# Kernel optimization log

Hardware: AMD Instinct MI355X
Metric: run time of the kernel (lower is better)

The kernel has to match this reference:

```python
import jax, jax.numpy as jnp
import numpy as np

N_NODES = 50000


def setup_inputs() -> dict:
    key = jax.random.key(0)
    k1, k2, k3, k4, k5 = jax.random.split(key, 5)
    h = jax.random.normal(k1, (50000, 256), dtype=jnp.float32)
    norm = jax.random.uniform(k2, (50000, 1), dtype=jnp.float32)
    weight = jax.random.normal(k3, (256, 96), dtype=jnp.float32) * (1.0 / np.sqrt(96.0))
    src = jax.random.randint(k4, (800000,), 0, N_NODES, dtype=jnp.int64)
    dst = jax.random.randint(k5, (800000,), 0, N_NODES, dtype=jnp.int64)
    return {"h": h, "norm": norm, "weight": weight, "src": src, "dst": dst}


def reference(h, norm, weight, src, dst):
    # dense projection: [N, in] @ [in, out] -> [N, out]
    hw = jnp.matmul(h, weight)
    # pre-aggregation degree norm
    hw = hw * norm
    # copy_src + sum: gather messages from src, scatter-add into dst
    msgs = hw[src]  # [E, out]
    agg = jax.ops.segment_sum(msgs, dst, num_segments=N_NODES)
    # post-aggregation degree norm + activation
    out = jax.nn.relu(agg * norm)
    return out
```

## Files before the change

### kernel.cpp

```cpp
#include <hip/hip_runtime.h>

#define M_NODES 50000
#define KDIM    256
#define NDIM    96
#define NEDGE   800000
#define BM      128
#define GEMM_BLKS 391
#define NPB     64
#define NBUCK   782
#define CAPB    1536
#define EPB     2048
#define NBLK_SC 391

typedef short bf16x8 __attribute__((ext_vector_type(8)));
typedef float f32x4  __attribute__((ext_vector_type(4)));

__device__ inline unsigned short f2bf(float x) {
    unsigned u = __float_as_uint(x);
    u = (u + 0x7fffu + ((u >> 16) & 1u)) >> 16;
    return (unsigned short)u;
}
__device__ inline unsigned pack2bf(float x, float y) {
    return (unsigned)f2bf(x) | ((unsigned)f2bf(y) << 16);
}

__global__ __launch_bounds__(256) void prep_w_kernel(
    const float* __restrict__ w, unsigned short* __restrict__ wt,
    int* __restrict__ gcursor)
{
    if (blockIdx.x == 0)
        for (int i = threadIdx.x; i < NBUCK; i += 256)
            gcursor[i] = i * CAPB;
    int i = blockIdx.x * 256 + threadIdx.x;
    if (i < KDIM * NDIM) {
        int n = i >> 8;
        int k = i & 255;
        wt[i] = f2bf(w[(size_t)k * NDIM + n]);
    }
}

__global__ __launch_bounds__(256) void fused_gemm_scatter_kernel(
    const float* __restrict__ h, const float* __restrict__ norm,
    const unsigned short* __restrict__ wt, unsigned short* __restrict__ hwb,
    const int* __restrict__ src, const int* __restrict__ dst,
    int* __restrict__ gcursor, unsigned* __restrict__ binned)
{
    __shared__ __align__(16) char smem[96 * 512];

    const int tid = threadIdx.x;

    if (blockIdx.x < GEMM_BLKS) {
        unsigned short* w_lds = reinterpret_cast<unsigned short*>(smem);
        const int lane = tid & 63;
        const int wv   = tid >> 6;
        const int row0 = blockIdx.x * BM;

#pragma unroll
        for (int it = 0; it < 12; ++it) {
            int idx = tid + it * 256;
            int n   = idx >> 5;
            int kb  = (idx & 31) * 16;
            uint4 v = *reinterpret_cast<const uint4*>(
                reinterpret_cast<const char*>(wt) + n * 512 + kb);
            *reinterpret_cast<uint4*>(
                reinterpret_cast<char*>(w_lds) + n * 512 + (kb ^ ((n & 7) << 4))) = v;
        }
        __syncthreads();

        f32x4 acc0[6], acc1[6];
#pragma unroll
        for (int f = 0; f < 6; ++f) {
            acc0[f] = (f32x4){0.f, 0.f, 0.f, 0.f};
            acc1[f] = (f32x4){0.f, 0.f, 0.f, 0.f};
        }

        const int ar = wv * 16 + (lane & 15);
        const int kg = lane >> 4;
        int arow0 = row0 + ar;
        int arow1 = row0 + ar + 64;
        if (arow0 >= M_NODES) arow0 = M_NODES - 1;
        if (arow1 >= M_NODES) arow1 = M_NODES - 1;
        const float* __restrict__ hr0 = h + (size_t)arow0 * KDIM;
        const float* __restrict__ hr1 = h + (size_t)arow1 * KDIM;

#pragma unroll
        for (int s = 0; s < 8; ++s) {
            const int k0 = s * 32 + kg * 8;
            float4 p0 = *reinterpret_cast<const float4*>(hr0 + k0);
            float4 q0 = *reinterpret_cast<const float4*>(hr0 + k0 + 4);
            float4 p1 = *reinterpret_cast<const float4*>(hr1 + k0);
            float4 q1 = *reinterpret_cast<const float4*>(hr1 + k0 + 4);
            union { bf16x8 v; unsigned u[4]; } a0, a1;
            a0.u[0] = pack2bf(p0.x, p0.y); a0.u[1] = pack2bf(p0.z, p0.w);
            a0.u[2] = pack2bf(q0.x, q0.y); a0.u[3] = pack2bf(q0.z, q0.w);
            a1.u[0] = pack2bf(p1.x, p1.y); a1.u[1] = pack2bf(p1.z, p1.w);
            a1.u[2] = pack2bf(q1.x, q1.y); a1.u[3] = pack2bf(q1.z, q1.w);

            const int kb = s * 64 + kg * 16;
#pragma unroll
            for (int f = 0; f < 6; ++f) {
                int n = f * 16 + (lane & 15);
                bf16x8 b = *reinterpret_cast<const bf16x8*>(
                    reinterpret_cast<const char*>(w_lds) + n * 512 + (kb ^ ((n & 7) << 4)));
                acc0[f] = __builtin_amdgcn_mfma_f32_16x16x32_bf16(a0.v, b, acc0[f], 0, 0, 0);
                acc1[f] = __builtin_amdgcn_mfma_f32_16x16x32_bf16(a1.v, b, acc1[f], 0, 0, 0);
            }
        }

        const int crow = wv * 16 + (lane >> 4) * 4;
        const int ccol = lane & 15;
#pragma unroll
        for (int r = 0; r < 4; ++r) {
            int rowA = row0 + crow + r;
            if (rowA < M_NODES) {
                float nv = norm[rowA];
#pragma unroll
                for (int f = 0; f < 6; ++f)
                    hwb[(size_t)rowA * NDIM + f * 16 + ccol] = f2bf(acc0[f][r] * nv);
            }
            int rowB = rowA + 64;
            if (rowB < M_NODES) {
                float nv = norm[rowB];
#pragma unroll
                for (int f = 0; f < 6; ++f)
                    hwb[(size_t)rowB * NDIM + f * 16 + ccol] = f2bf(acc1[f][r] * nv);
            }
        }
    } else {
        int* cnt  = reinterpret_cast<int*>(smem);
        int* base = cnt + NBUCK;
        const int blk = blockIdx.x - GEMM_BLKS;
        const int e0 = blk * EPB;
        const int e1 = (e0 + EPB < NEDGE) ? e0 + EPB : NEDGE;

        for (int i = tid; i < NBUCK; i += 256) cnt[i] = 0;
        __syncthreads();
        for (int e = e0 + tid; e < e1; e += 256)
            atomicAdd(&cnt[dst[e] >> 6], 1);
        __syncthreads();
        for (int i = tid; i < NBUCK; i += 256) {
            int c = cnt[i];
            base[i] = c ? atomicAdd(&gcursor[i], c) : 0;
        }
        __syncthreads();
        for (int i = tid; i < NBUCK; i += 256) cnt[i] = 0;
        __syncthreads();
        for (int e = e0 + tid; e < e1; e += 256) {
            int d = dst[e];
            int b = d >> 6;
            int pos = base[b] + atomicAdd(&cnt[b], 1);
            if (pos < (b + 1) * CAPB)
                binned[pos] = ((unsigned)(d & 63) << 16) | (unsigned)src[e];
        }
    }
}

#define ACCV(A, v)                                     \
    A[0] += __uint_as_float((v).x << 16);              \
    A[1] += __uint_as_float((v).x & 0xffff0000u);      \
    A[2] += __uint_as_float((v).y << 16);              \
    A[3] += __uint_as_float((v).y & 0xffff0000u);      \
    A[4] += __uint_as_float((v).z << 16);              \
    A[5] += __uint_as_float((v).z & 0xffff0000u);      \
    A[6] += __uint_as_float((v).w << 16);              \
    A[7] += __uint_as_float((v).w & 0xffff0000u);

__global__ __launch_bounds__(256) void csr_agg_kernel(
    const unsigned* __restrict__ binned, const int* __restrict__ gcursor,
    const unsigned short* __restrict__ hwb, const float* __restrict__ norm,
    float* __restrict__ out)
{
    __shared__ unsigned eL[CAPB];
    __shared__ unsigned short oL[CAPB];
    __shared__ int cnt[NPB];
    __shared__ int pfxE[NPB];

    const int b  = blockIdx.x;
    const int t  = threadIdx.x;
    const int e0 = b * CAPB;
    int cntE = gcursor[b] - e0;
    if (cntE > CAPB) cntE = CAPB;

    for (int i = t; i < cntE; i += 256) eL[i] = binned[e0 + i];
    if (t < NPB) cnt[t] = 0;
    __syncthreads();
    for (int i = t; i < cntE; i += 256)
        atomicAdd(&cnt[(eL[i] >> 16) & 63], 1);
    __syncthreads();
    if (t < NPB) pfxE[t] = cnt[t];
    __syncthreads();
    for (int st = 1; st < NPB; st <<= 1) {
        int o = (t >= st && t < NPB) ? pfxE[t - st] : 0;
        __syncthreads();
        if (t < NPB) pfxE[t] += o;
        __syncthreads();
    }
    if (t < NPB) {
        int ex = pfxE[t] - cnt[t];
        pfxE[t] = ex;
        cnt[t]  = ex;
    }
    __syncthreads();
    for (int i = t; i < cntE; i += 256) {
        unsigned v = eL[i];
        int d = (v >> 16) & 63;
        int p = atomicAdd(&cnt[d], 1);
        oL[p] = (unsigned short)(v & 0xffffu);
    }
    __syncthreads();

#pragma unroll
    for (int pass = 0; pass < 3; ++pass) {
        const int u     = pass * 256 + t;
        const int node  = u / 12;
        const int c8    = u - node * 12;
        const int gnode = b * NPB + node;
        if (gnode < M_NODES) {
            const int s0 = pfxE[node];
            const int s1 = cnt[node];
            float acc[8]  = {0.f, 0.f, 0.f, 0.f, 0.f, 0.f, 0.f, 0.f};
            float acc2[8] = {0.f, 0.f, 0.f, 0.f, 0.f, 0.f, 0.f, 0.f};
            int e = s0;
            for (; e + 4 <= s1; e += 4) {
                int a0 = oL[e], a1 = oL[e + 1], a2 = oL[e + 2], a3 = oL[e + 3];
                uint4 v0 = *reinterpret_cast<const uint4*>(hwb + (size_t)a0 * NDIM + c8 * 8);
                uint4 v1 = *reinterpret_cast<const uint4*>(hwb + (size_t)a1 * NDIM + c8 * 8);
                uint4 v2 = *reinterpret_cast<const uint4*>(hwb + (size_t)a2 * NDIM + c8 * 8);
                uint4 v3 = *reinterpret_cast<const uint4*>(hwb + (size_t)a3 * NDIM + c8 * 8);
                ACCV(acc, v0); ACCV(acc2, v1); ACCV(acc, v2); ACCV(acc2, v3);
            }
            for (; e < s1; ++e) {
                int a0 = oL[e];
                uint4 v0 = *reinterpret_cast<const uint4*>(hwb + (size_t)a0 * NDIM + c8 * 8);
                ACCV(acc, v0);
            }
            const float nv = norm[gnode];
            float4 o0, o1;
            o0.x = fmaxf((acc[0] + acc2[0]) * nv, 0.f);
            o0.y = fmaxf((acc[1] + acc2[1]) * nv, 0.f);
            o0.z = fmaxf((acc[2] + acc2[2]) * nv, 0.f);
            o0.w = fmaxf((acc[3] + acc2[3]) * nv, 0.f);
            o1.x = fmaxf((acc[4] + acc2[4]) * nv, 0.f);
            o1.y = fmaxf((acc[5] + acc2[5]) * nv, 0.f);
            o1.z = fmaxf((acc[6] + acc2[6]) * nv, 0.f);
            o1.w = fmaxf((acc[7] + acc2[7]) * nv, 0.f);
            float4* po = reinterpret_cast<float4*>(out + (size_t)gnode * NDIM + c8 * 8);
            po[0] = o0; po[1] = o1;
        }
    }
}

extern "C" void kernel_launch(void* const* d_in, const int* in_sizes, int n_in,
                              void* d_out, int out_size, void* d_ws, size_t ws_size,
                              hipStream_t stream)
{
    const float* h    = (const float*)d_in[0];
    const float* norm = (const float*)d_in[1];
    const float* w    = (const float*)d_in[2];
    const int*   src  = (const int*)d_in[3];
    const int*   dst  = (const int*)d_in[4];
    float* out = (float*)d_out;

    unsigned short* hwb = (unsigned short*)d_ws;
    unsigned short* wt  = hwb + (size_t)M_NODES * NDIM;
    int* gcursor = (int*)(wt + KDIM * NDIM);
    unsigned* binned = (unsigned*)(gcursor + 800);

    prep_w_kernel<<<(KDIM * NDIM + 255) / 256, 256, 0, stream>>>(w, wt, gcursor);
    fused_gemm_scatter_kernel<<<GEMM_BLKS + NBLK_SC, 256, 0, stream>>>(
        h, norm, wt, hwb, src, dst, gcursor, binned);
    csr_agg_kernel<<<NBUCK, 256, 0, stream>>>(binned, gcursor, hwb, norm, out);
}
```

Before: 70.36 us.

## Halve GEMM tile, read weights from global instead of LDS, shuffle-based prefix scan

The GEMM branch now processes 64 rows per block instead of 128 and launches twice as many GEMM blocks. It drops the LDS weight staging and syncthreads, reading bf16 weight fragments directly from global memory (L2/L1 cached). All h row loads are issued up front into registers. The binning branch gets smaller dedicated shared arrays, which may raise occupancy, and the aggregation kernel replaces the LDS/syncthreads Hillis-Steele scan with a single-wavefront __shfl_up scan. The trade-off is more global weight traffic per MFMA and less weight reuse per block.

```diff
diff --git a/kernel.cpp b/kernel.cpp
--- a/kernel.cpp
+++ b/kernel.cpp
@@ -4,8 +4,8 @@
 #define KDIM    256
 #define NDIM    96
 #define NEDGE   800000
-#define BM      128
-#define GEMM_BLKS 391
+#define BM      64
+#define GEMM_BLKS 782
 #define NPB     64
 #define NBUCK   782
 #define CAPB    1536
@@ -45,65 +45,48 @@
     const int* __restrict__ src, const int* __restrict__ dst,
     int* __restrict__ gcursor, unsigned* __restrict__ binned)
 {
-    __shared__ __align__(16) char smem[96 * 512];
+    __shared__ int s_cnt[NBUCK];
+    __shared__ int s_base[NBUCK];
 
     const int tid = threadIdx.x;
 
     if (blockIdx.x < GEMM_BLKS) {
-        unsigned short* w_lds = reinterpret_cast<unsigned short*>(smem);
         const int lane = tid & 63;
         const int wv   = tid >> 6;
         const int row0 = blockIdx.x * BM;
-
-#pragma unroll
-        for (int it = 0; it < 12; ++it) {
-            int idx = tid + it * 256;
-            int n   = idx >> 5;
-            int kb  = (idx & 31) * 16;
-            uint4 v = *reinterpret_cast<const uint4*>(
-                reinterpret_cast<const char*>(wt) + n * 512 + kb);
-            *reinterpret_cast<uint4*>(
-                reinterpret_cast<char*>(w_lds) + n * 512 + (kb ^ ((n & 7) << 4))) = v;
-        }
-        __syncthreads();
-
-        f32x4 acc0[6], acc1[6];
-#pragma unroll
-        for (int f = 0; f < 6; ++f) {
-            acc0[f] = (f32x4){0.f, 0.f, 0.f, 0.f};
-            acc1[f] = (f32x4){0.f, 0.f, 0.f, 0.f};
-        }
-
-        const int ar = wv * 16 + (lane & 15);
-        const int kg = lane >> 4;
-        int arow0 = row0 + ar;
-        int arow1 = row0 + ar + 64;
-        if (arow0 >= M_NODES) arow0 = M_NODES - 1;
-        if (arow1 >= M_NODES) arow1 = M_NODES - 1;
-        const float* __restrict__ hr0 = h + (size_t)arow0 * KDIM;
-        const float* __restrict__ hr1 = h + (size_t)arow1 * KDIM;
-
+        const int ar   = wv * 16 + (lane & 15);
+        const int kg   = lane >> 4;
+        int arow = row0 + ar;
+        if (arow >= M_NODES) arow = M_NODES - 1;
+        const float* __restrict__ hrow = h + (size_t)arow * KDIM + kg * 8;
+
+        float4 hr[16];
 #pragma unroll
         for (int s = 0; s < 8; ++s) {
-            const int k0 = s * 32 + kg * 8;
-            float4 p0 = *reinterpret_cast<const float4*>(hr0 + k0);
-            float4 q0 = *reinterpret_cast<const float4*>(hr0 + k0 + 4);
-            float4 p1 = *reinterpret_cast<const float4*>(hr1 + k0);
-            float4 q1 = *reinterpret_cast<const float4*>(hr1 + k0 + 4);
-            union { bf16x8 v; unsigned u[4]; } a0, a1;
-            a0.u[0] = pack2bf(p0.x, p0.y); a0.u[1] = pack2bf(p0.z, p0.w);
-            a0.u[2] = pack2bf(q0.x, q0.y); a0.u[3] = pack2bf(q0.z, q0.w);
-            a1.u[0] = pack2bf(p1.x, p1.y); a1.u[1] = pack2bf(p1.z, p1.w);
-            a1.u[2] = pack2bf(q1.x, q1.y); a1.u[3] = pack2bf(q1.z, q1.w);
-
-            const int kb = s * 64 + kg * 16;
+            hr[2 * s]     = *reinterpret_cast<const float4*>(hrow + s * 32);
+            hr[2 * s + 1] = *reinterpret_cast<const float4*>(hrow + s * 32 + 4);
+        }
+
+        const unsigned short* __restrict__ wb =
+            wt + (size_t)(lane & 15) * KDIM + kg * 8;
+
+        f32x4 acc[6];
+#pragma unroll
+        for (int f = 0; f < 6; ++f) acc[f] = (f32x4){0.f, 0.f, 0.f, 0.f};
+
+#pragma unroll
+        for (int s = 0; s < 8; ++s) {
+            union { bf16x8 v; unsigned u[4]; } a;
+            float4 p = hr[2 * s], q = hr[2 * s + 1];
+            a.u[0] = pack2bf(p.x, p.y);
+            a.u[1] = pack2bf(p.z, p.w);
+            a.u[2] = pack2bf(q.x, q.y);
+            a.u[3] = pack2bf(q.z, q.w);
 #pragma unroll
             for (int f = 0; f < 6; ++f) {
-                int n = f * 16 + (lane & 15);
                 bf16x8 b = *reinterpret_cast<const bf16x8*>(
-                    reinterpret_cast<const char*>(w_lds) + n * 512 + (kb ^ ((n & 7) << 4)));
-                acc0[f] = __builtin_amdgcn_mfma_f32_16x16x32_bf16(a0.v, b, acc0[f], 0, 0, 0);
-                acc1[f] = __builtin_amdgcn_mfma_f32_16x16x32_bf16(a1.v, b, acc1[f], 0, 0, 0);
+                    wb + (size_t)f * 16 * KDIM + s * 32);
+                acc[f] = __builtin_amdgcn_mfma_f32_16x16x32_bf16(a.v, b, acc[f], 0, 0, 0);
             }
         }
 
@@ -111,44 +94,35 @@
         const int ccol = lane & 15;
 #pragma unroll
         for (int r = 0; r < 4; ++r) {
-            int rowA = row0 + crow + r;
-            if (rowA < M_NODES) {
-                float nv = norm[rowA];
+            int row = row0 + crow + r;
+            if (row < M_NODES) {
+                float nv = norm[row];
 #pragma unroll
                 for (int f = 0; f < 6; ++f)
-                    hwb[(size_t)rowA * NDIM + f * 16 + ccol] = f2bf(acc0[f][r] * nv);
-            }
-            int rowB = rowA + 64;
-            if (rowB < M_NODES) {
-                float nv = norm[rowB];
-#pragma unroll
-                for (int f = 0; f < 6; ++f)
-                    hwb[(size_t)rowB * NDIM + f * 16 + ccol] = f2bf(acc1[f][r] * nv);
+                    hwb[(size_t)row * NDIM + f * 16 + ccol] = f2bf(acc[f][r] * nv);
             }
         }
     } else {
-        int* cnt  = reinterpret_cast<int*>(smem);
-        int* base = cnt + NBUCK;
         const int blk = blockIdx.x - GEMM_BLKS;
         const int e0 = blk * EPB;
         const int e1 = (e0 + EPB < NEDGE) ? e0 + EPB : NEDGE;
 
-        for (int i = tid; i < NBUCK; i += 256) cnt[i] = 0;
+        for (int i = tid; i < NBUCK; i += 256) s_cnt[i] = 0;
         __syncthreads();
         for (int e = e0 + tid; e < e1; e += 256)
-            atomicAdd(&cnt[dst[e] >> 6], 1);
+            atomicAdd(&s_cnt[dst[e] >> 6], 1);
         __syncthreads();
         for (int i = tid; i < NBUCK; i += 256) {
-            int c = cnt[i];
-            base[i] = c ? atomicAdd(&gcursor[i], c) : 0;
-        }
-        __syncthreads();
-        for (int i = tid; i < NBUCK; i += 256) cnt[i] = 0;
+            int c = s_cnt[i];
+            s_base[i] = c ? atomicAdd(&gcursor[i], c) : 0;
+        }
+        __syncthreads();
+        for (int i = tid; i < NBUCK; i += 256) s_cnt[i] = 0;
         __syncthreads();
         for (int e = e0 + tid; e < e1; e += 256) {
             int d = dst[e];
             int b = d >> 6;
-            int pos = base[b] + atomicAdd(&cnt[b], 1);
+            int pos = s_base[b] + atomicAdd(&s_cnt[b], 1);
             if (pos < (b + 1) * CAPB)
                 binned[pos] = ((unsigned)(d & 63) << 16) | (unsigned)src[e];
         }
@@ -187,16 +161,15 @@
     for (int i = t; i < cntE; i += 256)
         atomicAdd(&cnt[(eL[i] >> 16) & 63], 1);
     __syncthreads();
-    if (t < NPB) pfxE[t] = cnt[t];
-    __syncthreads();
-    for (int st = 1; st < NPB; st <<= 1) {
-        int o = (t >= st && t < NPB) ? pfxE[t - st] : 0;
-        __syncthreads();
-        if (t < NPB) pfxE[t] += o;
-        __syncthreads();
-    }
     if (t < NPB) {
-        int ex = pfxE[t] - cnt[t];
+        int v = cnt[t];
+        int x = v;
+#pragma unroll
+        for (int st = 1; st < 64; st <<= 1) {
+            int o = __shfl_up(x, st, 64);
+            if (t >= st) x += o;
+        }
+        int ex = x - v;
         pfxE[t] = ex;
         cnt[t]  = ex;
     }
```

New measurement: 81.00 us. 15.1% more time.
